# Kernel tuning notes

Measured on AMD Instinct MI355X. Metric: run time of the kernel, lower is better.

The kernel has to match this reference:

```python
import jax, jax.numpy as jnp
import numpy as np

D_X = D_Z = D_ATTN = D_OUT = 2048
L_Z = 32768


def setup_inputs() -> dict:
    key = jax.random.key(0)
    ks = jax.random.split(key, 8)
    xavier_q = (2.0 / (D_X + D_ATTN)) ** 0.5
    xavier_k = (2.0 / (D_Z + D_ATTN)) ** 0.5
    xavier_v = (2.0 / (D_Z + D_OUT)) ** 0.5
    return {
        "x": jax.random.normal(ks[0], (D_X,), jnp.float32),
        "zs": jax.random.normal(ks[1], (L_Z, D_Z), jnp.float32),
        "x_mask": 1,
        "zs_mask": jax.random.randint(ks[2], (L_Z,), 0, 2, jnp.int64.dtype if jax.config.read('jax_enable_x64') else jnp.int32),
        "w_q": jax.random.normal(ks[3], (D_X, D_ATTN), jnp.float32) * xavier_q,
        "w_k": jax.random.normal(ks[4], (D_Z, D_ATTN), jnp.float32) * xavier_k,
        "w_v": jax.random.normal(ks[5], (D_Z, D_OUT), jnp.float32) * xavier_v,
        "b_q": jnp.zeros((D_ATTN,), jnp.float32),
        "b_k": jnp.zeros((D_ATTN,), jnp.float32),
        "b_v": jnp.zeros((D_OUT,), jnp.float32),
    }


def reference(x, zs, x_mask, zs_mask, w_q, w_k, w_v, b_q, b_k, b_v):
    scale = 1.0 / jnp.sqrt(jnp.asarray(w_q.shape[1], x.dtype))
    q = x @ w_q + b_q                       # [d_attn]
    k = zs @ w_k + b_k                      # [l_z, d_attn]
    v = zs @ w_v + b_v                      # [l_z, d_out]
    score = (k @ q) * scale                 # [l_z]
    mask = (x_mask * zs_mask).astype(score.dtype)  # [l_z]
    bmask = mask != 0
    neg = jnp.finfo(score.dtype).min
    masked_score = jnp.where(bmask, score, neg)
    attention = jax.nn.softmax(masked_score, axis=-1) * mask  # [l_z]
    vt = attention @ v                      # [d_out] (vectorized form of the python loop)
    return (q, k, v, score, mask, masked_score, attention, vt)
```

## Files before the change

### kernel.cpp

```cpp
#include <hip/hip_runtime.h>
#include <hip/hip_bf16.h>
#include <cfloat>

#define DD   2048
#define LZ   32768

#define NEG_SENTINEL (-3.3895313892515355e38f)

typedef __bf16          bf16x8   __attribute__((ext_vector_type(8)));
typedef float           f32x4    __attribute__((ext_vector_type(4)));
typedef unsigned short  ushort8v __attribute__((ext_vector_type(8)));
typedef unsigned short  ushort4v __attribute__((ext_vector_type(4)));
typedef unsigned short  ushort_t;

typedef __attribute__((address_space(1))) const unsigned int guint_t;
typedef __attribute__((address_space(3))) unsigned int       luint_t;

__device__ __forceinline__ void gload16(const void* g, void* l) {
    __builtin_amdgcn_global_load_lds((guint_t*)g, (luint_t*)l, 16, 0, 0);
}

__device__ __forceinline__ unsigned short bf16_rne(float x) {
    unsigned u = __builtin_bit_cast(unsigned, x);
    u += 0x7fffu + ((u >> 16) & 1u);
    return (unsigned short)(u >> 16);
}

__device__ __forceinline__ void split_bf16(float x, unsigned short& hi, unsigned short& lo) {
    unsigned u = __builtin_bit_cast(unsigned, x);
    hi = (unsigned short)(u >> 16);
    float r = x - __builtin_bit_cast(float, u & 0xffff0000u);
    unsigned v = __builtin_bit_cast(unsigned, r);
    v += 0x7fffu + ((v >> 16) & 1u);
    lo = (unsigned short)(v >> 16);
}

#define TILE_US 8192

__global__ __launch_bounds__(256) void init_qvt(const float* __restrict__ b_q,
                                                float* __restrict__ q,
                                                float* __restrict__ vt) {
    int i = blockIdx.x * 256 + threadIdx.x;
    q[i]  = b_q[i];
    vt[i] = 0.0f;
}

__global__ __launch_bounds__(256) void q_gemv(const float* __restrict__ x,
                                              const float* __restrict__ w_q,
                                              float* __restrict__ q) {
    int n  = blockIdx.x * 256 + threadIdx.x;
    int c0 = blockIdx.y * 128;
    float acc = 0.0f;
    for (int c = 0; c < 128; ++c)
        acc = fmaf(x[c0 + c], w_q[(size_t)(c0 + c) * DD + n], acc);
    atomicAdd(&q[n], acc);
}

__global__ __launch_bounds__(256) void prea_kernel(const float* __restrict__ zs,
                                                   ushort_t* __restrict__ a_ws) {
    const int T = blockIdx.x;
    const int p = blockIdx.y;
    const int t = threadIdx.x;
    ushort_t* tile = a_ws + ((size_t)p * 32 + T) * TILE_US;
    #pragma unroll
    for (int j = 0; j < 4; ++j) {
        const int idx = t + j * 256;
        const int row = idx >> 3, k8 = idx & 7;
        const float4* src = (const float4*)(zs + ((size_t)p * 128 + row) * DD + T * 64 + k8 * 8);
        float4 f0 = src[0], f1 = src[1];
        ushort8v hv;
        hv[0] = bf16_rne(f0.x); hv[1] = bf16_rne(f0.y);
        hv[2] = bf16_rne(f0.z); hv[3] = bf16_rne(f0.w);
        hv[4] = bf16_rne(f1.x); hv[5] = bf16_rne(f1.y);
        hv[6] = bf16_rne(f1.z); hv[7] = bf16_rne(f1.w);
        const int phys = k8 ^ (row & 7);
        *(ushort8v*)(tile + (row * 8 + phys) * 8) = hv;
    }
}

__global__ __launch_bounds__(256) void preb_kernel(const float* __restrict__ w_k,
                                                   const float* __restrict__ w_v,
                                                   ushort_t* __restrict__ b_ws) {
    __shared__ float tile[64][65];
    const int mat = blockIdx.z;
    const float* w = mat ? w_v : w_k;
    const int T = blockIdx.x;
    const int kt0 = T * 64, nt0 = blockIdx.y * 64;
    const int t = threadIdx.x;
    const int rl  = t >> 4;
    const int cl4 = (t & 15) * 4;
    #pragma unroll
    for (int j = 0; j < 4; ++j) {
        float4 v4 = *(const float4*)&w[(size_t)(kt0 + rl + j * 16) * DD + nt0 + cl4];
        tile[rl + j * 16][cl4 + 0] = v4.x;
        tile[rl + j * 16][cl4 + 1] = v4.y;
        tile[rl + j * 16][cl4 + 2] = v4.z;
        tile[rl + j * 16][cl4 + 3] = v4.w;
    }
    __syncthreads();
    #pragma unroll
    for (int jj = 0; jj < 2; ++jj) {
        const int idx = t + jj * 256;
        const int n_l = idx >> 3, k8 = idx & 7;
        const int ng    = mat * DD + nt0 + n_l;
        const int panel = ng >> 7, prow = ng & 127;
        ushort8v hv;
        #pragma unroll
        for (int e = 0; e < 8; ++e)
            hv[e] = bf16_rne(tile[k8 * 8 + e][n_l]);
        ushort_t* dst = b_ws + ((size_t)panel * 32 + T) * TILE_US;
        const int phys = k8 ^ (prow & 7);
        *(ushort8v*)(dst + (prow * 8 + phys) * 8) = hv;
    }
}

__device__ __forceinline__ void phase_pre() {
    __builtin_amdgcn_s_barrier();
    asm volatile("s_waitcnt lgkmcnt(0)" ::: "memory");
    __builtin_amdgcn_sched_barrier(0);
    __builtin_amdgcn_s_setprio(1);
}
__device__ __forceinline__ void phase_post() {
    __builtin_amdgcn_s_setprio(0);
    __builtin_amdgcn_s_barrier();
}
__device__ __forceinline__ void vm_wait8() { asm volatile("s_waitcnt vmcnt(8)" ::: "memory"); }
__device__ __forceinline__ void vm_wait0() { asm volatile("s_waitcnt vmcnt(0)" ::: "memory"); }

__device__ __forceinline__ void kv_stage(const ushort_t* __restrict__ a_blk,
                                         const ushort_t* __restrict__ b_blk,
                                         char* LdsA, char* LdsB,
                                         int T, int wid, int lane) {
    const int p = T & 1;
    const bool isA = wid < 4;
    const int w4 = isA ? wid : wid - 4;
    const int h = w4 >> 1, qr = w4 & 1;
    const ushort_t* src = (isA ? a_blk : b_blk) + ((size_t)h * 32 + T) * TILE_US + qr * 4096;
    char* dst = (isA ? LdsA : LdsB) + p * 32768 + h * 16384 + qr * 8192;
    #pragma unroll
    for (int i = 0; i < 8; ++i) {
        const int g = i * 64 + lane;
        gload16(src + (size_t)g * 8, dst + g * 16);
    }
}

#define CLUSTER(AF, BF, R0)                                                              \
    {                                                                                    \
        _Pragma("unroll")                                                                \
        for (int i2 = 0; i2 < 4; ++i2) {                                                 \
            _Pragma("unroll")                                                            \
            for (int j = 0; j < 4; ++j)                                                  \
                acc[(R0) + i2][j] = __builtin_amdgcn_mfma_f32_16x16x32_bf16(             \
                    AF[i2], BF[j], acc[(R0) + i2][j], 0, 0, 0);                          \
        }                                                                                \
    }

#define LD8(dst, base, off)                                                              \
    dst = __builtin_bit_cast(bf16x8, *(const ushort8v*)((base) + (off)));

template<int TAIL>
__device__ __forceinline__ void kv_iter(
    const ushort_t* __restrict__ a_blk, const ushort_t* __restrict__ b_blk,
    char* LdsA, char* LdsB, int T,
    int wid, int lane, int wm, int wn,
    int soh, int sol, int arow, int brow,
    f32x4 (&acc)[8][4])
{
    const int p = T & 1;
    const char* Ab = LdsA + p * 32768 + wm * 16384;
    const char* Bb = LdsB + p * 32768 + (wn >> 1) * 16384;

    bf16x8 bu0[4], bu1[4], a0[4], a1[4], a2[4], a3[4];

    #pragma unroll
    for (int j = 0; j < 4; ++j) LD8(bu0[j], Bb, brow + j * 2048 + soh);
    #pragma unroll
    for (int i = 0; i < 4; ++i) LD8(a0[i], Ab, arow + i * 2048 + soh);
    phase_pre();
    CLUSTER(a0, bu0, 0);
    phase_post();

    #pragma unroll
    for (int i = 0; i < 4; ++i) LD8(a1[i], Ab, arow + (4 + i) * 2048 + soh);
    #pragma unroll
    for (int j = 0; j < 4; ++j) LD8(bu1[j], Bb, brow + j * 2048 + sol);
    phase_pre();
    CLUSTER(a1, bu0, 4);
    phase_post();

    #pragma unroll
    for (int i = 0; i < 4; ++i) LD8(a2[i], Ab, arow + i * 2048 + sol);
    #pragma unroll
    for (int i = 0; i < 4; ++i) LD8(a3[i], Ab, arow + (4 + i) * 2048 + sol);
    phase_pre();
    CLUSTER(a2, bu1, 0);
    phase_post();

    if (TAIL == 0) kv_stage(a_blk, b_blk, LdsA, LdsB, T + 2, wid, lane);
    if (TAIL == 0) vm_wait8();
    if (TAIL == 1) vm_wait0();
    phase_pre();
    CLUSTER(a3, bu1, 4);
    phase_post();
}

__global__ __launch_bounds__(512, 2)
void kv_gemm256(const ushort_t* __restrict__ a_ws, const ushort_t* __restrict__ b_ws,
                const float* __restrict__ b_k, const float* __restrict__ b_v,
                float* __restrict__ out_k, float* __restrict__ out_v)
{
    __shared__ char LdsA[2 * 32768];
    __shared__ char LdsB[2 * 32768];

    const int tid  = threadIdx.x;
    const int wid  = tid >> 6;
    const int lane = tid & 63;
    const int wm   = wid >> 2;
    const int wn   = wid & 3;
    const int lrow = lane & 15;
    const int lq   = lane >> 4;

    const int lin = blockIdx.x;
    const int swz = (lin & 7) * 256 + (lin >> 3);
    const int nb  = swz & 15;
    const int mb  = swz >> 4;

    const int m0   = mb * 256;
    const int n0   = nb * 256;
    const int mat  = n0 >> 11;
    const int nloc = n0 & (DD - 1);

    const ushort_t* a_blk = a_ws + (size_t)(mb * 2) * 32 * TILE_US;
    const ushort_t* b_blk = b_ws + (size_t)(nb * 2) * 32 * TILE_US;

    const int soh  = ((lq       ^ (lrow & 7)) << 4);
    const int sol  = (((lq | 4) ^ (lrow & 7)) << 4);
    const int arow = lrow * 128;
    const int brow = (wn & 1) * 8192 + lrow * 128;

    f32x4 acc[8][4] = {};

    kv_stage(a_blk, b_blk, LdsA, LdsB, 0, wid, lane);
    kv_stage(a_blk, b_blk, LdsA, LdsB, 1, wid, lane);
    vm_wait8();
    __builtin_amdgcn_sched_barrier(0);
    __builtin_amdgcn_s_barrier();

    for (int T = 0; T < 30; ++T)
        kv_iter<0>(a_blk, b_blk, LdsA, LdsB, T, wid, lane, wm, wn,
                   soh, sol, arow, brow, acc);
    kv_iter<1>(a_blk, b_blk, LdsA, LdsB, 30, wid, lane, wm, wn,
               soh, sol, arow, brow, acc);
    kv_iter<2>(a_blk, b_blk, LdsA, LdsB, 31, wid, lane, wm, wn,
               soh, sol, arow, brow, acc);

    const float* bias = mat ? b_v : b_k;
    float* outp = mat ? out_v : out_k;
    const int lq4 = lq * 4;
    #pragma unroll
    for (int j = 0; j < 4; ++j) {
        const int nout = nloc + wn * 64 + j * 16 + lrow;
        const float bv = bias[nout];
        #pragma unroll
        for (int i = 0; i < 8; ++i) {
            const int mbase = m0 + wm * 128 + i * 16 + lq4;
            #pragma unroll
            for (int r = 0; r < 4; ++r)
                outp[(size_t)(mbase + r) * DD + nout] = acc[i][j][r] + bv;
        }
    }
}

__global__ __launch_bounds__(256)
void kv_gemm_fb(const float* __restrict__ zs,
                const float* __restrict__ w_k, const float* __restrict__ w_v,
                const float* __restrict__ b_k, const float* __restrict__ b_v,
                float* __restrict__ out_k, float* __restrict__ out_v)
{
    __shared__ ushort_t As[128 * 64];
    __shared__ ushort_t Bs[128 * 64];

    const int tid  = threadIdx.x;
    const int m0   = blockIdx.y * 128;
    const int n0   = blockIdx.x * 128;
    const int mat  = n0 >> 11;
    const int nloc = n0 & (DD - 1);

    const int wid  = tid >> 6;
    const int lane = tid & 63;
    const int wm   = wid >> 1;
    const int wn   = wid & 1;
    const int lrow = lane & 15;
    const int lq   = lane >> 4;

    int aoff_hi[4], aoff_lo[4], boff_hi[4], boff_lo[4];
    #pragma unroll
    for (int i = 0; i < 4; ++i) {
        const int ra = wm * 64 + i * 16 + lrow;
        aoff_hi[i] = ra * 128 + ((lq       ^ (ra & 7)) * 16);
        aoff_lo[i] = ra * 128 + (((lq + 4) ^ (ra & 7)) * 16);
        const int rb = wn * 64 + i * 16 + lrow;
        boff_hi[i] = rb * 128 + ((lq       ^ (rb & 7)) * 16);
        boff_lo[i] = rb * 128 + (((lq + 4) ^ (rb & 7)) * 16);
    }

    f32x4 acc[4][4] = {};
    const int srow  = tid >> 1;
    const int shalf = tid & 1;

    for (int ks = 0; ks < 64; ++ks) {
        {
            const float4* ap = (const float4*)(zs + (size_t)(m0 + srow) * DD + ks * 32 + shalf * 16);
            float4 f0 = ap[0], f1 = ap[1], f2 = ap[2], f3 = ap[3];
            float e[16] = {f0.x,f0.y,f0.z,f0.w, f1.x,f1.y,f1.z,f1.w,
                           f2.x,f2.y,f2.z,f2.w, f3.x,f3.y,f3.z,f3.w};
            ushort8v h0, h1, l0, l1;
            #pragma unroll
            for (int c = 0; c < 8; ++c) {
                unsigned short hh, ll;
                split_bf16(e[c], hh, ll);
                h0[c] = hh; l0[c] = ll;
                split_bf16(e[8 + c], hh, ll);
                h1[c] = hh; l1[c] = ll;
            }
            char* rowbase = (char*)As + srow * 128;
            const int s0 = (shalf * 2)     ^ (srow & 7);
            const int s1 = (shalf * 2 + 1) ^ (srow & 7);
            *(ushort8v*)(rowbase + s0 * 16)       = h0;
            *(ushort8v*)(rowbase + s1 * 16)       = h1;
            *(ushort8v*)(rowbase + (s0 ^ 4) * 16) = l0;
            *(ushort8v*)(rowbase + (s1 ^ 4) * 16) = l1;
        }
        {
            const float* w = mat ? w_v : w_k;
            const int k_l = (tid >> 5) * 4;
            const int n_l = (tid & 31) * 4;
            float4 r0 = *(const float4*)&w[(size_t)(ks * 32 + k_l + 0) * DD + nloc + n_l];
            float4 r1 = *(const float4*)&w[(size_t)(ks * 32 + k_l + 1) * DD + nloc + n_l];
            float4 r2 = *(const float4*)&w[(size_t)(ks * 32 + k_l + 2) * DD + nloc + n_l];
            float4 r3 = *(const float4*)&w[(size_t)(ks * 32 + k_l + 3) * DD + nloc + n_l];
            float el[4][4] = {{r0.x,r0.y,r0.z,r0.w},{r1.x,r1.y,r1.z,r1.w},
                              {r2.x,r2.y,r2.z,r2.w},{r3.x,r3.y,r3.z,r3.w}};
            const int slot = k_l >> 3, sub = ((k_l >> 2) & 1) * 8;
            #pragma unroll
            for (int c = 0; c < 4; ++c) {
                const int n = n_l + c;
                ushort4v hv, lv;
                #pragma unroll
                for (int r = 0; r < 4; ++r) {
                    unsigned short hh, ll;
                    split_bf16(el[r][c], hh, ll);
                    hv[r] = hh; lv[r] = ll;
                }
                char* rb = (char*)Bs + n * 128;
                const int sp = slot ^ (n & 7);
                *(ushort4v*)(rb + sp * 16 + sub)       = hv;
                *(ushort4v*)(rb + (sp ^ 4) * 16 + sub) = lv;
            }
        }
        __syncthreads();

        bf16x8 a_hi[4], a_lo[4], b_hi[4], b_lo[4];
        #pragma unroll
        for (int i = 0; i < 4; ++i) {
            a_hi[i] = __builtin_bit_cast(bf16x8, *(const ushort8v*)((const char*)As + aoff_hi[i]));
            a_lo[i] = __builtin_bit_cast(bf16x8, *(const ushort8v*)((const char*)As + aoff_lo[i]));
            b_hi[i] = __builtin_bit_cast(bf16x8, *(const ushort8v*)((const char*)Bs + boff_hi[i]));
            b_lo[i] = __builtin_bit_cast(bf16x8, *(const ushort8v*)((const char*)Bs + boff_lo[i]));
        }
        #pragma unroll
        for (int i = 0; i < 4; ++i)
            #pragma unroll
            for (int j = 0; j < 4; ++j)
                acc[i][j] = __builtin_amdgcn_mfma_f32_16x16x32_bf16(a_hi[i], b_hi[j], acc[i][j], 0, 0, 0);
        #pragma unroll
        for (int i = 0; i < 4; ++i)
            #pragma unroll
            for (int j = 0; j < 4; ++j)
                acc[i][j] = __builtin_amdgcn_mfma_f32_16x16x32_bf16(a_hi[i], b_lo[j], acc[i][j], 0, 0, 0);
        #pragma unroll
        for (int i = 0; i < 4; ++i)
            #pragma unroll
            for (int j = 0; j < 4; ++j)
                acc[i][j] = __builtin_amdgcn_mfma_f32_16x16x32_bf16(a_lo[i], b_hi[j], acc[i][j], 0, 0, 0);
        __syncthreads();
    }

    const float* bias = mat ? b_v : b_k;
    float* outp = mat ? out_v : out_k;
    #pragma unroll
    for (int j = 0; j < 4; ++j) {
        const int nout = nloc + wn * 64 + j * 16 + lrow;
        const float bv = bias[nout];
        #pragma unroll
        for (int i = 0; i < 4; ++i) {
            const int mbase = m0 + wm * 64 + i * 16 + lq * 4;
            #pragma unroll
            for (int r = 0; r < 4; ++r)
                outp[(size_t)(mbase + r) * DD + nout] = acc[i][j][r] + bv;
        }
    }
}

__global__ __launch_bounds__(256) void score_kernel(const float* __restrict__ k,
                                                    const float* __restrict__ q,
                                                    const int* __restrict__ x_mask,
                                                    const int* __restrict__ zs_mask,
                                                    float* __restrict__ score,
                                                    float* __restrict__ maskout,
                                                    float* __restrict__ masked) {
    const int wid = threadIdx.x >> 6, lane = threadIdx.x & 63;
    const int l = blockIdx.x * 4 + wid;
    const float4* krow = (const float4*)(k + (size_t)l * DD);
    const float4* q4   = (const float4*)q;
    float acc = 0.0f;
    #pragma unroll
    for (int it = 0; it < 8; ++it) {
        float4 kv = krow[lane + it * 64];
        float4 qv = q4[lane + it * 64];
        acc = fmaf(kv.x, qv.x, acc);
        acc = fmaf(kv.y, qv.y, acc);
        acc = fmaf(kv.z, qv.z, acc);
        acc = fmaf(kv.w, qv.w, acc);
    }
    #pragma unroll
    for (int off = 32; off; off >>= 1) acc += __shfl_xor(acc, off, 64);
    if (lane == 0) {
        float s = acc * 0.022097086912079608f;
        float m = (float)(x_mask[0] * zs_mask[l]);
        score[l]   = s;
        maskout[l] = m;
        masked[l]  = (m != 0.0f) ? s : NEG_SENTINEL;
    }
}

__global__ __launch_bounds__(1024) void softmax_kernel(const float* __restrict__ masked,
                                                       const float* __restrict__ maskv,
                                                       float* __restrict__ attention) {
    __shared__ float red[16];
    __shared__ float gsh[2];
    const int t = threadIdx.x;
    const int wid = t >> 6, lane = t & 63;

    float mx = -FLT_MAX;
    for (int i = t; i < LZ; i += 1024) mx = fmaxf(mx, masked[i]);
    #pragma unroll
    for (int off = 32; off; off >>= 1) mx = fmaxf(mx, __shfl_xor(mx, off, 64));
    if (lane == 0) red[wid] = mx;
    __syncthreads();
    if (t == 0) {
        float g = red[0];
        for (int i = 1; i < 16; ++i) g = fmaxf(g, red[i]);
        gsh[0] = g;
    }
    __syncthreads();
    const float gmax = gsh[0];

    float s = 0.0f;
    for (int i = t; i < LZ; i += 1024) s += expf(masked[i] - gmax);
    #pragma unroll
    for (int off = 32; off; off >>= 1) s += __shfl_xor(s, off, 64);
    if (lane == 0) red[wid] = s;
    __syncthreads();
    if (t == 0) {
        float g = 0.0f;
        for (int i = 0; i < 16; ++i) g += red[i];
        gsh[1] = g;
    }
    __syncthreads();
    const float inv = 1.0f / gsh[1];

    for (int i = t; i < LZ; i += 1024)
        attention[i] = expf(masked[i] - gmax) * inv * maskv[i];
}

__global__ __launch_bounds__(256) void vt_kernel(const float* __restrict__ v,
                                                 const float* __restrict__ attention,
                                                 float* __restrict__ vt) {
    __shared__ float att_s[512];
    const int t = threadIdx.x;
    const int d = blockIdx.x * 256 + t;
    const int l0 = blockIdx.y * 512;
    att_s[t]       = attention[l0 + t];
    att_s[t + 256] = attention[l0 + t + 256];
    __syncthreads();
    float acc = 0.0f;
    const float* vp = v + (size_t)l0 * DD + d;
    for (int i = 0; i < 512; ++i)
        acc = fmaf(att_s[i], vp[(size_t)i * DD], acc);
    atomicAdd(&vt[d], acc);
}

extern "C" void kernel_launch(void* const* d_in, const int* in_sizes, int n_in,
                              void* d_out, int out_size, void* d_ws, size_t ws_size,
                              hipStream_t stream) {
    const float* x       = (const float*)d_in[0];
    const float* zs      = (const float*)d_in[1];
    const int*   x_mask  = (const int*)d_in[2];
    const int*   zs_mask = (const int*)d_in[3];
    const float* w_q     = (const float*)d_in[4];
    const float* w_k     = (const float*)d_in[5];
    const float* w_v     = (const float*)d_in[6];
    const float* b_q     = (const float*)d_in[7];
    const float* b_k     = (const float*)d_in[8];
    const float* b_v     = (const float*)d_in[9];

    float* out       = (float*)d_out;
    float* q         = out;
    float* k         = q + DD;
    float* v         = k + (size_t)LZ * DD;
    float* score     = v + (size_t)LZ * DD;
    float* maskv     = score + LZ;
    float* masked    = maskv + LZ;
    float* attention = masked + LZ;
    float* vt        = attention + LZ;

    init_qvt<<<8, 256, 0, stream>>>(b_q, q, vt);
    q_gemv<<<dim3(8, 16), 256, 0, stream>>>(x, w_q, q);

    const size_t A_WS = (size_t)256 * 32 * TILE_US * sizeof(ushort_t);
    const size_t B_WS = (size_t)32  * 32 * TILE_US * sizeof(ushort_t);

    if (ws_size >= A_WS + B_WS) {
        ushort_t* a_ws = (ushort_t*)d_ws;
        ushort_t* b_ws = (ushort_t*)((char*)d_ws + A_WS);
        prea_kernel<<<dim3(32, 256), 256, 0, stream>>>(zs, a_ws);
        preb_kernel<<<dim3(32, 32, 2), 256, 0, stream>>>(w_k, w_v, b_ws);
        kv_gemm256<<<2048, 512, 0, stream>>>(a_ws, b_ws, b_k, b_v, k, v);
    } else {
        kv_gemm_fb<<<dim3(32, 256), 256, 0, stream>>>(zs, w_k, w_v, b_k, b_v, k, v);
    }

    score_kernel<<<8192, 256, 0, stream>>>(k, q, x_mask, zs_mask, score, maskv, masked);
    softmax_kernel<<<1, 1024, 0, stream>>>(masked, maskv, attention);
    vt_kernel<<<dim3(8, 64), 256, 0, stream>>>(v, attention, vt);
}
```

Baseline: 858.3 us.

## Software-pipeline LDS fragment loads across K-iterations in KV GEMM

Restructures the KV GEMM inner loop so the first A/B fragments for the next tile are read from LDS during the last MFMA cluster of the current tile. Partial lgkmcnt waits replace the full waits, so each cluster's LDS reads overlap the preceding cluster's MFMAs. The aim is to hide LDS latency at phase boundaries. In exchange, the global prefetch now waits for vmcnt(0) every iteration instead of vmcnt(8), which may expose global-load latency, and carrying fragments across iterations raises register pressure.

```diff
diff --git a/kernel.cpp b/kernel.cpp
--- a/kernel.cpp
+++ b/kernel.cpp
@@ -114,16 +114,6 @@
     }
 }
 
-__device__ __forceinline__ void phase_pre() {
-    __builtin_amdgcn_s_barrier();
-    asm volatile("s_waitcnt lgkmcnt(0)" ::: "memory");
-    __builtin_amdgcn_sched_barrier(0);
-    __builtin_amdgcn_s_setprio(1);
-}
-__device__ __forceinline__ void phase_post() {
-    __builtin_amdgcn_s_setprio(0);
-    __builtin_amdgcn_s_barrier();
-}
 __device__ __forceinline__ void vm_wait8() { asm volatile("s_waitcnt vmcnt(8)" ::: "memory"); }
 __device__ __forceinline__ void vm_wait0() { asm volatile("s_waitcnt vmcnt(0)" ::: "memory"); }
 
@@ -158,50 +148,74 @@
 #define LD8(dst, base, off)                                                              \
     dst = __builtin_bit_cast(bf16x8, *(const ushort8v*)((base) + (off)));
 
+#define LGKM(N)  asm volatile("s_waitcnt lgkmcnt(" #N ")" ::: "memory")
+
 template<int TAIL>
 __device__ __forceinline__ void kv_iter(
     const ushort_t* __restrict__ a_blk, const ushort_t* __restrict__ b_blk,
     char* LdsA, char* LdsB, int T,
     int wid, int lane, int wm, int wn,
     int soh, int sol, int arow, int brow,
+    bf16x8 (&a0)[4], bf16x8 (&b0)[4],
     f32x4 (&acc)[8][4])
 {
     const int p = T & 1;
     const char* Ab = LdsA + p * 32768 + wm * 16384;
     const char* Bb = LdsB + p * 32768 + (wn >> 1) * 16384;
 
-    bf16x8 bu0[4], bu1[4], a0[4], a1[4], a2[4], a3[4];
-
-    #pragma unroll
-    for (int j = 0; j < 4; ++j) LD8(bu0[j], Bb, brow + j * 2048 + soh);
-    #pragma unroll
-    for (int i = 0; i < 4; ++i) LD8(a0[i], Ab, arow + i * 2048 + soh);
-    phase_pre();
-    CLUSTER(a0, bu0, 0);
-    phase_post();
+    bf16x8 a1[4], a2[4], a3[4], b1[4];
 
     #pragma unroll
     for (int i = 0; i < 4; ++i) LD8(a1[i], Ab, arow + (4 + i) * 2048 + soh);
-    #pragma unroll
-    for (int j = 0; j < 4; ++j) LD8(bu1[j], Bb, brow + j * 2048 + sol);
-    phase_pre();
-    CLUSTER(a1, bu0, 4);
-    phase_post();
+    __builtin_amdgcn_s_barrier();
+    LGKM(4);
+    __builtin_amdgcn_sched_barrier(0);
+    __builtin_amdgcn_s_setprio(1);
+    CLUSTER(a0, b0, 0);
+    __builtin_amdgcn_s_setprio(0);
+    __builtin_amdgcn_s_barrier();
 
     #pragma unroll
     for (int i = 0; i < 4; ++i) LD8(a2[i], Ab, arow + i * 2048 + sol);
     #pragma unroll
+    for (int j = 0; j < 4; ++j) LD8(b1[j], Bb, brow + j * 2048 + sol);
+    __builtin_amdgcn_s_barrier();
+    LGKM(8);
+    __builtin_amdgcn_sched_barrier(0);
+    __builtin_amdgcn_s_setprio(1);
+    CLUSTER(a1, b0, 4);
+    __builtin_amdgcn_s_setprio(0);
+    __builtin_amdgcn_s_barrier();
+
+    #pragma unroll
     for (int i = 0; i < 4; ++i) LD8(a3[i], Ab, arow + (4 + i) * 2048 + sol);
-    phase_pre();
-    CLUSTER(a2, bu1, 0);
-    phase_post();
-
+    __builtin_amdgcn_s_barrier();
+    LGKM(4);
+    __builtin_amdgcn_sched_barrier(0);
+    __builtin_amdgcn_s_setprio(1);
+    CLUSTER(a2, b1, 0);
+    __builtin_amdgcn_s_setprio(0);
+    __builtin_amdgcn_s_barrier();
+
+    LGKM(0);
+    if (TAIL <= 1) vm_wait0();
+    __builtin_amdgcn_sched_barrier(0);
+    __builtin_amdgcn_s_barrier();
+    if (TAIL <= 1) {
+        const int np = (T + 1) & 1;
+        const char* Abn = LdsA + np * 32768 + wm * 16384;
+        const char* Bbn = LdsB + np * 32768 + (wn >> 1) * 16384;
+        #pragma unroll
+        for (int i = 0; i < 4; ++i) LD8(a0[i], Abn, arow + i * 2048 + soh);
+        #pragma unroll
+        for (int j = 0; j < 4; ++j) LD8(b0[j], Bbn, brow + j * 2048 + soh);
+    }
     if (TAIL == 0) kv_stage(a_blk, b_blk, LdsA, LdsB, T + 2, wid, lane);
-    if (TAIL == 0) vm_wait8();
-    if (TAIL == 1) vm_wait0();
-    phase_pre();
-    CLUSTER(a3, bu1, 4);
-    phase_post();
+    __builtin_amdgcn_sched_barrier(0);
+    __builtin_amdgcn_s_setprio(1);
+    CLUSTER(a3, b1, 4);
+    __builtin_amdgcn_s_setprio(0);
+    __builtin_amdgcn_s_barrier();
 }
 
 __global__ __launch_bounds__(512, 2)
@@ -239,20 +253,29 @@
     const int brow = (wn & 1) * 8192 + lrow * 128;
 
     f32x4 acc[8][4] = {};
+    bf16x8 a0[4], b0[4];
 
     kv_stage(a_blk, b_blk, LdsA, LdsB, 0, wid, lane);
     kv_stage(a_blk, b_blk, LdsA, LdsB, 1, wid, lane);
     vm_wait8();
     __builtin_amdgcn_sched_barrier(0);
     __builtin_amdgcn_s_barrier();
+    {
+        const char* Ab0 = LdsA + wm * 16384;
+        const char* Bb0 = LdsB + (wn >> 1) * 16384;
+        #pragma unroll
+        for (int i = 0; i < 4; ++i) LD8(a0[i], Ab0, arow + i * 2048 + soh);
+        #pragma unroll
+        for (int j = 0; j < 4; ++j) LD8(b0[j], Bb0, brow + j * 2048 + soh);
+    }
 
     for (int T = 0; T < 30; ++T)
         kv_iter<0>(a_blk, b_blk, LdsA, LdsB, T, wid, lane, wm, wn,
-                   soh, sol, arow, brow, acc);
+                   soh, sol, arow, brow, a0, b0, acc);
     kv_iter<1>(a_blk, b_blk, LdsA, LdsB, 30, wid, lane, wm, wn,
-               soh, sol, arow, brow, acc);
+               soh, sol, arow, brow, a0, b0, acc);
     kv_iter<2>(a_blk, b_blk, LdsA, LdsB, 31, wid, lane, wm, wn,
-               soh, sol, arow, brow, acc);
+               soh, sol, arow, brow, a0, b0, acc);
 
     const float* bias = mat ? b_v : b_k;
     float* outp = mat ? out_v : out_k;
```

Measured after the change: 825.3 us. -3.9%, faster.
